# Kernel tuning notes

Hardware: AMD Instinct MI355X
Metric: run time of the kernel (lower is better)

The kernel has to match this reference:

```python
import jax, jax.numpy as jnp
import numpy as np

S, B, NINP, NHID, NLAYERS = 512, 128, 128, 128, 3


def setup_inputs() -> dict:
    key = jax.random.key(0)
    ks = jax.random.split(key, 6)
    stdv = 1.0 / float(np.sqrt(NHID))
    u = lambda k, shape: jax.random.uniform(k, shape, jnp.float32, -stdv, stdv)
    return {
        "x": jax.random.normal(ks[0], (S, B, NINP), jnp.float32),
        "lin_w": u(ks[1], (NHID, NINP)),
        "lin_b": u(ks[2], (NHID,)),
        "W": u(ks[3], (NLAYERS, 4 * NHID, NHID)),
        "U": u(ks[4], (NLAYERS, 4 * NHID, NLAYERS * NHID)),
        "G": u(ks[5], (NLAYERS, NHID, 1)),
    }


def reference(x, lin_w, lin_b, W, U, G):
    # x: [S, B, ninp]; eval mode (no dropout masks), feedback=True, gated=True.
    S_, B_, _ = x.shape
    L = W.shape[0]
    H = W.shape[1] // 4
    xp = x @ lin_w.T + lin_b  # [S, B, H] input projection
    h0 = jnp.zeros((L, B_, H), x.dtype)
    c0 = jnp.zeros((L, B_, H), x.dtype)

    def step(carry, xt):
        h, c = carry  # each [L, B, H]
        # gated: per-layer scalar sigmoid gate, broadcast over H
        gh = jax.nn.sigmoid(jnp.einsum('lbh,lho->lbo', h, G))  # [L, B, 1]
        h = gh * h
        # feedback: concat all layers' hidden along features, shared by every layer
        hx = h.transpose(1, 0, 2).reshape(B_, L * H)  # [B, L*H]
        inp = xt  # [B, H]; stacked layers: output of layer i feeds layer i+1
        hs, cs = [], []
        for i in range(L):
            gates = inp @ W[i].T + hx @ U[i].T  # [B, 4H]
            ig, fg, gg, og = jnp.split(gates, 4, axis=-1)
            ig = jax.nn.sigmoid(ig)
            fg = jax.nn.sigmoid(fg)
            gg = jnp.tanh(gg)
            og = jax.nn.sigmoid(og)
            cy = fg * c[i] + ig * gg
            hy = og * jnp.tanh(cy)
            hs.append(hy)
            cs.append(cy)
            inp = hy
        return (jnp.stack(hs, 0), jnp.stack(cs, 0)), None

    (h, c), _ = jax.lax.scan(step, (h0, c0), xp)
    return (h, c)
```

## Files before the change

kernel.cpp:

```cpp
#include <hip/hip_runtime.h>

#define S_LEN 512
#define BATCH 128
#define NH    128
#define NL    3

#define HXS  392
#define INPS 136

#define XP_OFF   0u
#define WP_OFF   16777216u
#define UP_OFF   (WP_OFF + 393216u)
#define HX_OFF   (UP_OFF + 1179648u)
#define FLAG_OFF (HX_OFF + 196608u)
#define FLAG_SZ  49152u

typedef float f32x4 __attribute__((ext_vector_type(4)));
typedef short bf16x8 __attribute__((ext_vector_type(8)));
typedef unsigned long long u64;

__device__ __forceinline__ short f2bf(float f) {
    unsigned u = __builtin_bit_cast(unsigned, f);
    u = (u + 0x7FFFu + ((u >> 16) & 1u)) >> 16;
    return (short)u;
}
__device__ __forceinline__ float bf2f_lo(unsigned u) { return __builtin_bit_cast(float, u << 16); }
__device__ __forceinline__ float bf2f_hi(unsigned u) { return __builtin_bit_cast(float, u & 0xFFFF0000u); }
__device__ __forceinline__ float sigm(float x) { return 1.f / (1.f + __expf(-x)); }
__device__ __forceinline__ float tanh_fast(float x) { return 2.f / (1.f + __expf(-2.f * x)) - 1.f; }

__global__ __launch_bounds__(128) void xp_kernel(const float* __restrict__ x,
        const float* __restrict__ lin_w, const float* __restrict__ lin_b,
        short* __restrict__ xp) {
    __shared__ float xs[8 * 128];
    const int tid = threadIdx.x;
    const long r0 = (long)blockIdx.x * 8;
    for (int rr = 0; rr < 8; ++rr)
        xs[rr * 128 + tid] = x[(r0 + rr) * 128 + tid];
    __syncthreads();
    float acc[8];
    float bias = lin_b[tid];
    #pragma unroll
    for (int rr = 0; rr < 8; ++rr) acc[rr] = bias;
    const float* wrow = lin_w + (long)tid * 128;
    for (int k = 0; k < 128; ++k) {
        float wv = wrow[k];
        #pragma unroll
        for (int rr = 0; rr < 8; ++rr) acc[rr] += xs[rr * 128 + k] * wv;
    }
    for (int rr = 0; rr < 8; ++rr)
        xp[(r0 + rr) * 128 + tid] = f2bf(acc[rr]);
}

__global__ __launch_bounds__(256) void pack_kernel(const float* __restrict__ W,
        const float* __restrict__ U, short* __restrict__ Wp, short* __restrict__ Up) {
    int id = blockIdx.x * 256 + threadIdx.x;
    int lane = id & 63;
    int fid = id >> 6;
    int lr = lane & 15, lk = lane >> 4;
    if (fid < 384) {
        int kt = fid & 3, g = (fid >> 2) & 3, unit = fid >> 4;
        int l = unit >> 3, c = unit & 7;
        int row = g * 128 + c * 16 + lr;
        const float* src = W + ((long)(l * 512 + row)) * 128 + kt * 32 + lk * 8;
        short* dst = Wp + (long)fid * 512 + lane * 8;
        #pragma unroll
        for (int j = 0; j < 8; ++j) dst[j] = f2bf(src[j]);
    } else {
        int f = fid - 384;
        int kt = f % 12, gu = f / 12;
        int g = gu & 3, unit = gu >> 2;
        int l = unit >> 3, c = unit & 7;
        int row = g * 128 + c * 16 + lr;
        const float* src = U + ((long)(l * 512 + row)) * 384 + kt * 32 + lk * 8;
        short* dst = Up + (long)f * 512 + lane * 8;
        #pragma unroll
        for (int j = 0; j < 8; ++j) dst[j] = f2bf(src[j]);
    }
}

__global__ __launch_bounds__(256, 1) void lstm_kernel(
    const short* __restrict__ xp, const short* __restrict__ Wp,
    const short* __restrict__ Up, const float* __restrict__ Gp,
    unsigned* __restrict__ hexch, unsigned* __restrict__ flags,
    float* __restrict__ out)
{
    __shared__ short hx_lds[16 * HXS];
    __shared__ short inp_lds[16 * INPS];
    __shared__ float gates_lds[4 * 16 * 17];
    __shared__ float G_lds[NL * 128];
    __shared__ short hsl[16 * 16];
    __shared__ int s_abort;

    const int tid  = threadIdx.x;
    const int lane = tid & 63;
    const int w    = tid >> 6;
    const int lr   = lane & 15;
    const int lk   = lane >> 4;
    const int grp  = blockIdx.x & 7;
    const int unit = blockIdx.x >> 3;
    const int l    = unit >> 3;
    const int c    = unit & 7;
    const int b0   = grp * 16;
    const int bb   = tid >> 4;
    const int nn   = tid & 15;

    u64* hexch64 = (u64*)hexch;

    bf16x8 ufr[12], wfr[4];
    {
        const short* ub = Up + ((long)(unit * 4 + w) * 12) * 512 + lane * 8;
        #pragma unroll
        for (int kt = 0; kt < 12; ++kt) ufr[kt] = *(const bf16x8*)(ub + kt * 512);
        const short* wb = Wp + ((long)(unit * 4 + w) * 4) * 512 + lane * 8;
        #pragma unroll
        for (int kt = 0; kt < 4; ++kt) wfr[kt] = *(const bf16x8*)(wb + kt * 512);
    }
    #pragma unroll
    for (int kt = 0; kt < 12; ++kt) asm volatile("" : "+v"(ufr[kt]));
    #pragma unroll
    for (int kt = 0; kt < 4; ++kt)  asm volatile("" : "+v"(wfr[kt]));

    for (int i = tid; i < NL * 128; i += 256) G_lds[i] = Gp[i];
    if (tid == 0) s_abort = 0;
    float c_reg = 0.f;
    __syncthreads();

    for (int t = 0; t < S_LEN; ++t) {
        const int par  = t & 1;
        const int ppar = par ^ 1;

        bf16x8 xa[4];
        if (l == 0) {
            const short* xp_t = xp + ((long)t * BATCH + b0) * 128;
            #pragma unroll
            for (int kt = 0; kt < 4; ++kt)
                xa[kt] = *(const bf16x8*)(xp_t + lr * 128 + kt * 32 + lk * 8);
        }

        if (t == 0) {
            for (int i = tid; i < 16 * HXS; i += 256) hx_lds[i] = 0;
        } else if (w < 3) {
            {
                const unsigned fidx = ((unsigned)(t - 1) * 3 + w) * 8 + grp;
                int g = 0;
                while (__hip_atomic_load(&flags[fidx], __ATOMIC_RELAXED, __HIP_MEMORY_SCOPE_AGENT) < 8u) {
                    if (*(volatile int*)&s_abort) break;
                    if (++g > 300000) { *(volatile int*)&s_abort = 1; break; }
                }
            }
            const int p = lane >> 2, sub = lane & 3;
            const u64* src64 = hexch64 + (unsigned)(ppar * 8 + grp) * 1536
                             + (unsigned)(w * 16 + p) * 32 + sub * 8;
            u64 hv[8];
            #pragma unroll
            for (int k = 0; k < 8; ++k)
                hv[k] = __hip_atomic_load(&src64[k], __ATOMIC_RELAXED, __HIP_MEMORY_SCOPE_AGENT);
            const float* gbase = &G_lds[w * 128 + sub * 32];
            float s = 0.f;
            #pragma unroll
            for (int k = 0; k < 8; ++k) {
                unsigned lo = (unsigned)hv[k], hi = (unsigned)(hv[k] >> 32);
                s += bf2f_lo(lo) * gbase[4 * k + 0];
                s += bf2f_hi(lo) * gbase[4 * k + 1];
                s += bf2f_lo(hi) * gbase[4 * k + 2];
                s += bf2f_hi(hi) * gbase[4 * k + 3];
            }
            s += __shfl_xor(s, 1, 64);
            s += __shfl_xor(s, 2, 64);
            float gh = sigm(s);
            #pragma unroll
            for (int k = 0; k < 8; ++k) {
                unsigned lo = (unsigned)hv[k], hi = (unsigned)(hv[k] >> 32);
                unsigned r0 = (unsigned)(unsigned short)f2bf(gh * bf2f_lo(lo))
                            | ((unsigned)(unsigned short)f2bf(gh * bf2f_hi(lo)) << 16);
                unsigned r1 = (unsigned)(unsigned short)f2bf(gh * bf2f_lo(hi))
                            | ((unsigned)(unsigned short)f2bf(gh * bf2f_hi(hi)) << 16);
                *(u64*)&hx_lds[p * HXS + w * 128 + sub * 32 + 4 * k] =
                    ((u64)r1 << 32) | (u64)r0;
            }
        }
        __syncthreads();

        f32x4 acc = (f32x4){0.f, 0.f, 0.f, 0.f};
        #pragma unroll
        for (int kt = 0; kt < 12; ++kt) {
            bf16x8 a = *(const bf16x8*)&hx_lds[lr * HXS + kt * 32 + lk * 8];
            acc = __builtin_amdgcn_mfma_f32_16x16x32_bf16(a, ufr[kt], acc, 0, 0, 0);
        }

        if (l == 0) {
            #pragma unroll
            for (int kt = 0; kt < 4; ++kt)
                acc = __builtin_amdgcn_mfma_f32_16x16x32_bf16(xa[kt], wfr[kt], acc, 0, 0, 0);
        } else {
            {
                const unsigned fidx = ((unsigned)t * 3 + (l - 1)) * 8 + grp;
                int g = 0;
                while (__hip_atomic_load(&flags[fidx], __ATOMIC_RELAXED, __HIP_MEMORY_SCOPE_AGENT) < 8u) {
                    if (*(volatile int*)&s_abort) break;
                    if (++g > 300000) { *(volatile int*)&s_abort = 1; break; }
                }
            }
            const u64* isrc64 = hexch64 + (unsigned)(par * 8 + grp) * 1536 + (unsigned)((l - 1) * 16) * 32;
            #pragma unroll
            for (int rep = 0; rep < 2; ++rep) {
                int i = tid + rep * 256;
                int bi = i >> 5, kq = i & 31;
                u64 u = __hip_atomic_load(&isrc64[i], __ATOMIC_RELAXED, __HIP_MEMORY_SCOPE_AGENT);
                *(u64*)&inp_lds[bi * INPS + 4 * kq] = u;
            }
            __syncthreads();
            #pragma unroll
            for (int kt = 0; kt < 4; ++kt) {
                bf16x8 a = *(const bf16x8*)&inp_lds[lr * INPS + kt * 32 + lk * 8];
                acc = __builtin_amdgcn_mfma_f32_16x16x32_bf16(a, wfr[kt], acc, 0, 0, 0);
            }
        }

        #pragma unroll
        for (int r = 0; r < 4; ++r)
            gates_lds[w * 272 + (lk * 4 + r) * 17 + lr] = acc[r];
        __syncthreads();

        float ig = sigm(gates_lds[0 * 272 + bb * 17 + nn]);
        float fg = sigm(gates_lds[1 * 272 + bb * 17 + nn]);
        float gg = tanh_fast(gates_lds[2 * 272 + bb * 17 + nn]);
        float og = sigm(gates_lds[3 * 272 + bb * 17 + nn]);
        float cn = fg * c_reg + ig * gg;
        c_reg = cn;
        float hy = og * tanh_fast(cn);
        hsl[bb * 16 + nn] = f2bf(hy);
        if (t == S_LEN - 1) {
            long o = ((long)(l * BATCH + b0 + bb)) * NH + c * 16 + nn;
            out[o] = hy;
            out[(long)NL * BATCH * NH + o] = cn;
        }
        __syncthreads();

        if (tid < 64) {
            int row = tid >> 2, q = tid & 3;
            u64 v = ((const u64*)hsl)[tid];
            u64* dst = hexch64 + (unsigned)(par * 8 + grp) * 1536
                     + (unsigned)(l * 16 + row) * 32 + c * 4 + q;
            __hip_atomic_store(dst, v, __ATOMIC_RELAXED, __HIP_MEMORY_SCOPE_AGENT);
            asm volatile("s_waitcnt vmcnt(0)" ::: "memory");
            if (tid == 0)
                __hip_atomic_fetch_add(&flags[((unsigned)t * 3 + l) * 8 + grp], 1u,
                                       __ATOMIC_RELAXED, __HIP_MEMORY_SCOPE_AGENT);
        }
    }
}

extern "C" void kernel_launch(void* const* d_in, const int* in_sizes, int n_in,
                              void* d_out, int out_size, void* d_ws, size_t ws_size,
                              hipStream_t stream) {
    const float* x     = (const float*)d_in[0];
    const float* lin_w = (const float*)d_in[1];
    const float* lin_b = (const float*)d_in[2];
    const float* W     = (const float*)d_in[3];
    const float* U     = (const float*)d_in[4];
    const float* G     = (const float*)d_in[5];
    float* out = (float*)d_out;

    short*    xp    = (short*)((char*)d_ws + XP_OFF);
    short*    Wp    = (short*)((char*)d_ws + WP_OFF);
    short*    Up    = (short*)((char*)d_ws + UP_OFF);
    unsigned* hexch = (unsigned*)((char*)d_ws + HX_OFF);
    unsigned* flags = (unsigned*)((char*)d_ws + FLAG_OFF);

    hipMemsetAsync(flags, 0, FLAG_SZ, stream);
    hipLaunchKernelGGL(xp_kernel,   dim3(8192), dim3(128), 0, stream, x, lin_w, lin_b, xp);
    hipLaunchKernelGGL(pack_kernel, dim3(384),  dim3(256), 0, stream, W, U, Wp, Up);
    hipLaunchKernelGGL(lstm_kernel, dim3(192),  dim3(256), 0, stream,
                       xp, Wp, Up, G, hexch, flags, out);
}
```

Baseline: 3.901 ms.

## Replace flag counters with sequence-tagged 16-byte packets for hidden-state exchange

Drops the separate per-step atomic flag counters and their spin loops. Each 16-byte store now carries six bf16 values plus the step number in its last dword, and consumers poll the data itself with cache-bypassing loads until every tag matches. This removes the store, wait, atomic-add, poll chain from the inter-block critical path. It also splits the MFMA accumulation into two independent accumulators to shorten dependency chains. In exchange the exchange buffer grows by a third, and ordering correctness relies on 16-byte stores landing atomically.

```diff
diff --git a/kernel.cpp b/kernel.cpp
--- a/kernel.cpp
+++ b/kernel.cpp
@@ -12,11 +12,11 @@
 #define WP_OFF   16777216u
 #define UP_OFF   (WP_OFF + 393216u)
 #define HX_OFF   (UP_OFF + 1179648u)
-#define FLAG_OFF (HX_OFF + 196608u)
-#define FLAG_SZ  49152u
+#define HX_SZ    294912u
 
 typedef float f32x4 __attribute__((ext_vector_type(4)));
 typedef short bf16x8 __attribute__((ext_vector_type(8)));
+typedef unsigned u32x4 __attribute__((ext_vector_type(4)));
 typedef unsigned long long u64;
 
 __device__ __forceinline__ short f2bf(float f) {
@@ -79,18 +79,17 @@
     }
 }
 
+
 __global__ __launch_bounds__(256, 1) void lstm_kernel(
     const short* __restrict__ xp, const short* __restrict__ Wp,
     const short* __restrict__ Up, const float* __restrict__ Gp,
-    unsigned* __restrict__ hexch, unsigned* __restrict__ flags,
-    float* __restrict__ out)
+    char* __restrict__ hexch, float* __restrict__ out)
 {
     __shared__ short hx_lds[16 * HXS];
     __shared__ short inp_lds[16 * INPS];
     __shared__ float gates_lds[4 * 16 * 17];
     __shared__ float G_lds[NL * 128];
     __shared__ short hsl[16 * 16];
-    __shared__ int s_abort;
 
     const int tid  = threadIdx.x;
     const int lane = tid & 63;
@@ -105,8 +104,6 @@
     const int bb   = tid >> 4;
     const int nn   = tid & 15;
 
-    u64* hexch64 = (u64*)hexch;
-
     bf16x8 ufr[12], wfr[4];
     {
         const short* ub = Up + ((long)(unit * 4 + w) * 12) * 512 + lane * 8;
@@ -122,9 +119,11 @@
     for (int kt = 0; kt < 4; ++kt)  asm volatile("" : "+v"(wfr[kt]));
 
     for (int i = tid; i < NL * 128; i += 256) G_lds[i] = Gp[i];
-    if (tid == 0) s_abort = 0;
     float c_reg = 0.f;
     __syncthreads();
+
+    const int offs[6] = {0, 6, 12, 16, 22, 28};
+    const int nw[6]   = {3, 3, 2, 3, 3, 2};
 
     for (int t = 0; t < S_LEN; ++t) {
         const int par  = t & 1;
@@ -141,86 +140,121 @@
         if (t == 0) {
             for (int i = tid; i < 16 * HXS; i += 256) hx_lds[i] = 0;
         } else if (w < 3) {
-            {
-                const unsigned fidx = ((unsigned)(t - 1) * 3 + w) * 8 + grp;
-                int g = 0;
-                while (__hip_atomic_load(&flags[fidx], __ATOMIC_RELAXED, __HIP_MEMORY_SCOPE_AGENT) < 8u) {
-                    if (*(volatile int*)&s_abort) break;
-                    if (++g > 300000) { *(volatile int*)&s_abort = 1; break; }
-                }
-            }
             const int p = lane >> 2, sub = lane & 3;
-            const u64* src64 = hexch64 + (unsigned)(ppar * 8 + grp) * 1536
-                             + (unsigned)(w * 16 + p) * 32 + sub * 8;
-            u64 hv[8];
-            #pragma unroll
-            for (int k = 0; k < 8; ++k)
-                hv[k] = __hip_atomic_load(&src64[k], __ATOMIC_RELAXED, __HIP_MEMORY_SCOPE_AGENT);
-            const float* gbase = &G_lds[w * 128 + sub * 32];
+            const unsigned want = (unsigned)t;
+            const u64 abase = (u64)(hexch + (size_t)(((ppar * 8 + grp) * 3 + w)) * 6144
+                                          + ((size_t)p * 24 + sub * 6) * 16);
+            u32x4 q0, q1, q2, q3, q4, q5;
+            for (int rounds = 0;; ++rounds) {
+                asm volatile(
+                    "global_load_dwordx4 %0, %6, off sc0 sc1\n\t"
+                    "global_load_dwordx4 %1, %6, off offset:16 sc0 sc1\n\t"
+                    "global_load_dwordx4 %2, %6, off offset:32 sc0 sc1\n\t"
+                    "global_load_dwordx4 %3, %6, off offset:48 sc0 sc1\n\t"
+                    "global_load_dwordx4 %4, %6, off offset:64 sc0 sc1\n\t"
+                    "global_load_dwordx4 %5, %6, off offset:80 sc0 sc1\n\t"
+                    "s_waitcnt vmcnt(0)"
+                    : "=&v"(q0), "=&v"(q1), "=&v"(q2), "=&v"(q3), "=&v"(q4), "=&v"(q5)
+                    : "v"(abase) : "memory");
+                bool fresh = (q0[3] == want) && (q1[3] == want) && (q2[3] == want)
+                          && (q3[3] == want) && (q4[3] == want) && (q5[3] == want);
+                if (__all(fresh) || rounds > 262144) break;
+            }
+            const float* gb = &G_lds[w * 128 + sub * 32];
             float s = 0.f;
-            #pragma unroll
-            for (int k = 0; k < 8; ++k) {
-                unsigned lo = (unsigned)hv[k], hi = (unsigned)(hv[k] >> 32);
-                s += bf2f_lo(lo) * gbase[4 * k + 0];
-                s += bf2f_hi(lo) * gbase[4 * k + 1];
-                s += bf2f_lo(hi) * gbase[4 * k + 2];
-                s += bf2f_hi(hi) * gbase[4 * k + 3];
-            }
+            u32x4 qs[6] = {q0, q1, q2, q3, q4, q5};
+            #pragma unroll
+            for (int k = 0; k < 6; ++k)
+                #pragma unroll
+                for (int i = 0; i < 3; ++i)
+                    if (i < nw[k]) {
+                        unsigned wd = qs[k][i];
+                        s += bf2f_lo(wd) * gb[offs[k] + 2 * i]
+                           + bf2f_hi(wd) * gb[offs[k] + 2 * i + 1];
+                    }
             s += __shfl_xor(s, 1, 64);
             s += __shfl_xor(s, 2, 64);
             float gh = sigm(s);
             #pragma unroll
-            for (int k = 0; k < 8; ++k) {
-                unsigned lo = (unsigned)hv[k], hi = (unsigned)(hv[k] >> 32);
-                unsigned r0 = (unsigned)(unsigned short)f2bf(gh * bf2f_lo(lo))
-                            | ((unsigned)(unsigned short)f2bf(gh * bf2f_hi(lo)) << 16);
-                unsigned r1 = (unsigned)(unsigned short)f2bf(gh * bf2f_lo(hi))
-                            | ((unsigned)(unsigned short)f2bf(gh * bf2f_hi(hi)) << 16);
-                *(u64*)&hx_lds[p * HXS + w * 128 + sub * 32 + 4 * k] =
-                    ((u64)r1 << 32) | (u64)r0;
-            }
+            for (int k = 0; k < 6; ++k)
+                #pragma unroll
+                for (int i = 0; i < 3; ++i)
+                    if (i < nw[k]) {
+                        unsigned wd = qs[k][i];
+                        unsigned r = (unsigned)(unsigned short)f2bf(gh * bf2f_lo(wd))
+                                   | ((unsigned)(unsigned short)f2bf(gh * bf2f_hi(wd)) << 16);
+                        *(unsigned*)&hx_lds[p * HXS + w * 128 + sub * 32 + offs[k] + 2 * i] = r;
+                    }
         }
         __syncthreads();
 
-        f32x4 acc = (f32x4){0.f, 0.f, 0.f, 0.f};
+        f32x4 acc0 = (f32x4){0.f, 0.f, 0.f, 0.f};
+        f32x4 acc1 = (f32x4){0.f, 0.f, 0.f, 0.f};
         #pragma unroll
         for (int kt = 0; kt < 12; ++kt) {
             bf16x8 a = *(const bf16x8*)&hx_lds[lr * HXS + kt * 32 + lk * 8];
-            acc = __builtin_amdgcn_mfma_f32_16x16x32_bf16(a, ufr[kt], acc, 0, 0, 0);
+            if (kt & 1) acc1 = __builtin_amdgcn_mfma_f32_16x16x32_bf16(a, ufr[kt], acc1, 0, 0, 0);
+            else        acc0 = __builtin_amdgcn_mfma_f32_16x16x32_bf16(a, ufr[kt], acc0, 0, 0, 0);
         }
 
         if (l == 0) {
             #pragma unroll
-            for (int kt = 0; kt < 4; ++kt)
-                acc = __builtin_amdgcn_mfma_f32_16x16x32_bf16(xa[kt], wfr[kt], acc, 0, 0, 0);
+            for (int kt = 0; kt < 4; ++kt) {
+                if (kt & 1) acc1 = __builtin_amdgcn_mfma_f32_16x16x32_bf16(xa[kt], wfr[kt], acc1, 0, 0, 0);
+                else        acc0 = __builtin_amdgcn_mfma_f32_16x16x32_bf16(xa[kt], wfr[kt], acc0, 0, 0, 0);
+            }
         } else {
+            const unsigned want = (unsigned)(t + 1);
+            const u64 base = (u64)(hexch + (size_t)(((par * 8 + grp) * 3 + (l - 1))) * 6144);
+            const int ch0 = tid;
+            const u64 a0 = base + (size_t)ch0 * 16;
+            const u64 a1 = a0 + 4096;
+            u32x4 q0, q1;
+            if (tid < 128) {
+                for (int rounds = 0;; ++rounds) {
+                    asm volatile(
+                        "global_load_dwordx4 %0, %2, off sc0 sc1\n\t"
+                        "global_load_dwordx4 %1, %3, off sc0 sc1\n\t"
+                        "s_waitcnt vmcnt(0)"
+                        : "=&v"(q0), "=&v"(q1) : "v"(a0), "v"(a1) : "memory");
+                    if (__all((q0[3] == want) && (q1[3] == want)) || rounds > 262144) break;
+                }
+            } else {
+                for (int rounds = 0;; ++rounds) {
+                    asm volatile(
+                        "global_load_dwordx4 %0, %1, off sc0 sc1\n\t"
+                        "s_waitcnt vmcnt(0)"
+                        : "=&v"(q0) : "v"(a0) : "memory");
+                    if (__all(q0[3] == want) || rounds > 262144) break;
+                }
+            }
             {
-                const unsigned fidx = ((unsigned)t * 3 + (l - 1)) * 8 + grp;
-                int g = 0;
-                while (__hip_atomic_load(&flags[fidx], __ATOMIC_RELAXED, __HIP_MEMORY_SCOPE_AGENT) < 8u) {
-                    if (*(volatile int*)&s_abort) break;
-                    if (++g > 300000) { *(volatile int*)&s_abort = 1; break; }
+                int row = ch0 / 24, m = ch0 % 24, cc = m / 3, j = m % 3;
+                int sbase = row * INPS + cc * 16 + 6 * j;
+                *(unsigned*)&inp_lds[sbase] = q0[0];
+                *(unsigned*)&inp_lds[sbase + 2] = q0[1];
+                if (j < 2) *(unsigned*)&inp_lds[sbase + 4] = q0[2];
+                if (tid < 128) {
+                    int ch1 = ch0 + 256;
+                    int row1 = ch1 / 24, m1 = ch1 % 24, c1 = m1 / 3, j1 = m1 % 3;
+                    int sb1 = row1 * INPS + c1 * 16 + 6 * j1;
+                    *(unsigned*)&inp_lds[sb1] = q1[0];
+                    *(unsigned*)&inp_lds[sb1 + 2] = q1[1];
+                    if (j1 < 2) *(unsigned*)&inp_lds[sb1 + 4] = q1[2];
                 }
-            }
-            const u64* isrc64 = hexch64 + (unsigned)(par * 8 + grp) * 1536 + (unsigned)((l - 1) * 16) * 32;
-            #pragma unroll
-            for (int rep = 0; rep < 2; ++rep) {
-                int i = tid + rep * 256;
-                int bi = i >> 5, kq = i & 31;
-                u64 u = __hip_atomic_load(&isrc64[i], __ATOMIC_RELAXED, __HIP_MEMORY_SCOPE_AGENT);
-                *(u64*)&inp_lds[bi * INPS + 4 * kq] = u;
             }
             __syncthreads();
             #pragma unroll
             for (int kt = 0; kt < 4; ++kt) {
                 bf16x8 a = *(const bf16x8*)&inp_lds[lr * INPS + kt * 32 + lk * 8];
-                acc = __builtin_amdgcn_mfma_f32_16x16x32_bf16(a, wfr[kt], acc, 0, 0, 0);
+                if (kt & 1) acc1 = __builtin_amdgcn_mfma_f32_16x16x32_bf16(a, wfr[kt], acc1, 0, 0, 0);
+                else        acc0 = __builtin_amdgcn_mfma_f32_16x16x32_bf16(a, wfr[kt], acc0, 0, 0, 0);
             }
         }
 
         #pragma unroll
         for (int r = 0; r < 4; ++r)
-            gates_lds[w * 272 + (lk * 4 + r) * 17 + lr] = acc[r];
+            gates_lds[w * 272 + (lk * 4 + r) * 17 + lr] = acc0[r] + acc1[r];
         __syncthreads();
 
         float ig = sigm(gates_lds[0 * 272 + bb * 17 + nn]);
@@ -238,16 +272,16 @@
         }
         __syncthreads();
 
-        if (tid < 64) {
-            int row = tid >> 2, q = tid & 3;
-            u64 v = ((const u64*)hsl)[tid];
-            u64* dst = hexch64 + (unsigned)(par * 8 + grp) * 1536
-                     + (unsigned)(l * 16 + row) * 32 + c * 4 + q;
-            __hip_atomic_store(dst, v, __ATOMIC_RELAXED, __HIP_MEMORY_SCOPE_AGENT);
-            asm volatile("s_waitcnt vmcnt(0)" ::: "memory");
-            if (tid == 0)
-                __hip_atomic_fetch_add(&flags[((unsigned)t * 3 + l) * 8 + grp], 1u,
-                                       __ATOMIC_RELAXED, __HIP_MEMORY_SCOPE_AGENT);
+        if (tid < 48) {
+            int row = tid / 3, j = tid % 3;
+            const unsigned* hslw = (const unsigned*)hsl;
+            unsigned d0, d1, d2;
+            if (j < 2) { d0 = hslw[row * 8 + 3 * j]; d1 = hslw[row * 8 + 3 * j + 1]; d2 = hslw[row * 8 + 3 * j + 2]; }
+            else       { d0 = hslw[row * 8 + 6];     d1 = hslw[row * 8 + 7];         d2 = 0; }
+            u32x4 dq = (u32x4){d0, d1, d2, (unsigned)(t + 1)};
+            u64 pa = (u64)(hexch + (size_t)(((par * 8 + grp) * 3 + l)) * 6144
+                                 + ((size_t)row * 24 + c * 3 + j) * 16);
+            asm volatile("global_store_dwordx4 %0, %1, off sc0 sc1" :: "v"(pa), "v"(dq) : "memory");
         }
     }
 }
@@ -263,15 +297,14 @@
     const float* G     = (const float*)d_in[5];
     float* out = (float*)d_out;
 
-    short*    xp    = (short*)((char*)d_ws + XP_OFF);
-    short*    Wp    = (short*)((char*)d_ws + WP_OFF);
-    short*    Up    = (short*)((char*)d_ws + UP_OFF);
-    unsigned* hexch = (unsigned*)((char*)d_ws + HX_OFF);
-    unsigned* flags = (unsigned*)((char*)d_ws + FLAG_OFF);
-
-    hipMemsetAsync(flags, 0, FLAG_SZ, stream);
+    short* xp    = (short*)((char*)d_ws + XP_OFF);
+    short* Wp    = (short*)((char*)d_ws + WP_OFF);
+    short* Up    = (short*)((char*)d_ws + UP_OFF);
+    char*  hexch = (char*)d_ws + HX_OFF;
+
+    hipMemsetAsync(hexch, 0, HX_SZ, stream);
     hipLaunchKernelGGL(xp_kernel,   dim3(8192), dim3(128), 0, stream, x, lin_w, lin_b, xp);
     hipLaunchKernelGGL(pack_kernel, dim3(384),  dim3(256), 0, stream, W, U, Wp, Up);
     hipLaunchKernelGGL(lstm_kernel, dim3(192),  dim3(256), 0, stream,
-                       xp, Wp, Up, G, hexch, flags, out);
-}
+                       xp, Wp, Up, G, hexch, out);
+}
```

Result: slower. 4.058 ms (+4.0%).
